# Optimization experiments

Measured on AMD Instinct MI355X. Metric: run time of the kernel, lower is better.

The kernel has to match this reference:

```python
import jax, jax.numpy as jnp
import numpy as np

N = 8192      # nodes; also input feature dim (x.shape[0] used as in_channels)
E = 524288    # edges per edge type (avg degree 64)
H = 200       # hidden dim (hard-coded in RecomNet)
MEAN_RATING = 3.5


def setup_inputs() -> dict:
    key = jax.random.key(0)
    ks = jax.random.split(key, 14)
    s_in = np.float32(1.0 / np.sqrt(N))
    s_h = np.float32(1.0 / np.sqrt(H))
    return {
        "x": jax.random.normal(ks[0], (N, N), jnp.float32),
        "edge_sim": jax.random.randint(ks[1], (2, E), 0, N),
        "edge_rat": jax.random.randint(ks[2], (2, E), 0, N),
        "mask": jax.random.randint(ks[3], (E,), 0, 2).astype(bool),
        # conv1 params (in=N, out=H)
        "w1_self": jax.random.normal(ks[4], (N, H), jnp.float32) * s_in,
        "w1_sim": jax.random.normal(ks[5], (N, H), jnp.float32) * s_in,
        "w1_rat": jax.random.normal(ks[6], (N, H), jnp.float32) * s_in,
        "b1": jnp.zeros((H,), jnp.float32),
        # conv2 params (in=H, out=H)
        "w2_self": jax.random.normal(ks[7], (H, H), jnp.float32) * s_h,
        "w2_sim": jax.random.normal(ks[8], (H, H), jnp.float32) * s_h,
        "w2_rat": jax.random.normal(ks[9], (H, H), jnp.float32) * s_h,
        "b2": jnp.zeros((H,), jnp.float32),
        # bilinear decoder
        "Q": jax.random.normal(ks[10], (H, H), jnp.float32) * s_h,
    }


def _recom_conv(edge_sim, edge_rat, x, w_self, w_sim, w_rat, b):
    # linear-then-gather-then-scatter (linear commutes with sum aggregation)
    m_sim = (x @ w_sim)[edge_sim[0]]                                   # [E, H]
    agg_sim = jax.ops.segment_sum(m_sim, edge_sim[1], num_segments=N)  # [N, H]
    m_rat = (x @ w_rat)[edge_rat[0]]
    agg_rat = jax.ops.segment_sum(m_rat, edge_rat[1], num_segments=N)
    return x @ w_self + agg_sim + agg_rat + b


def reference(x, w1_self, w1_sim, w1_rat, b1, w2_self, w2_sim, w2_rat, b2, Q,
              edge_sim, edge_rat, mask):
    h = _recom_conv(edge_sim, edge_rat, x, w1_self, w1_sim, w1_rat, b1)
    h = jax.nn.relu(h)
    h = _recom_conv(edge_sim, edge_rat, h, w2_self, w2_sim, w2_rat, b2)
    h1 = h[edge_rat[0]]                                                # [E, H]
    h2 = h[edge_rat[1]]                                                # [E, H]
    pred = jnp.einsum("eh,hk,ek->e", h1, Q, h2) + MEAN_RATING          # [E]
    # original compacts with boolean mask (dynamic shape); here we keep a
    # fixed [E] output and zero out unmasked edges
    return jnp.where(mask, pred, 0.0)
```

## Files before the change

### kernel.cpp

```cpp
#include <hip/hip_runtime.h>

#define NN 8192
#define EE 524288
#define HPAD 256
#define NP 640
#define PSS ((size_t)NN * 200)
#define PSM ((size_t)NN * 400)

using s16x8 = __attribute__((ext_vector_type(8))) short;
using u16x8 = __attribute__((ext_vector_type(8))) unsigned short;
using f32x4 = __attribute__((ext_vector_type(4))) float;

__device__ __forceinline__ unsigned short f2b(float f) {
    unsigned u = __float_as_uint(f);
    u = (u + 0x7FFFu + ((u >> 16) & 1u)) >> 16;
    return (unsigned short)u;
}
__device__ __forceinline__ float b2f(unsigned short u) {
    return __uint_as_float((unsigned)u << 16);
}
__device__ __forceinline__ unsigned pkbf16(float a, float b) {
    unsigned r;
    asm("v_cvt_pk_bf16_f32 %0, %1, %2" : "=v"(r) : "v"(a), "v"(b));
    return r;
}

__device__ __forceinline__ void async16(const unsigned short* g, unsigned short* l)
{
    __builtin_amdgcn_global_load_lds(
        (const __attribute__((address_space(1))) unsigned int*)g,
        (__attribute__((address_space(3))) unsigned int*)l, 16, 0, 0);
}

__global__ void transpose_w_kernel(
    const float* __restrict__ u0, const float* __restrict__ u1,
    const float* __restrict__ u2,
    const float* __restrict__ v0, const float* __restrict__ v1,
    const float* __restrict__ v2,
    const float* __restrict__ Q,
    unsigned short* __restrict__ o0, unsigned short* __restrict__ o1,
    unsigned short* __restrict__ o2)
{
    const int zc = blockIdx.z;
    const float *w0, *w1, *w2;
    unsigned short* out;
    int Kout, Kreal, Nreal;
    if (zc == 0)      { w0 = u0; w1 = u1; w2 = u2; out = o0; Kout = NN;   Kreal = NN;  Nreal = 600; }
    else if (zc == 1) { w0 = v0; w1 = v1; w2 = v2; out = o1; Kout = HPAD; Kreal = 200; Nreal = 600; }
    else              { w0 = Q;  w1 = Q;  w2 = Q;  out = o2; Kout = HPAD; Kreal = 200; Nreal = 200; }
    const int kb = blockIdx.x << 5;
    const int nb = blockIdx.y << 5;
    if (kb >= Kout) return;
    __shared__ float tile[32][33];
    const int tx = threadIdx.x, ty = threadIdx.y;
    const int n = nb + tx;
    const float* w = (n < 200) ? w0 : (n < 400) ? w1 : w2;
    const int c = (n < 200) ? n : (n < 400) ? n - 200 : n - 400;
#pragma unroll
    for (int i = 0; i < 4; ++i) {
        const int k = kb + ty + (i << 3);
        float v = 0.f;
        if (n < Nreal && k < Kreal) v = w[(size_t)k * 200 + c];
        tile[ty + (i << 3)][tx] = v;
    }
    __syncthreads();
#pragma unroll
    for (int i = 0; i < 4; ++i) {
        const int nn = nb + ty + (i << 3);
        out[(size_t)nn * Kout + kb + tx] = f2b(tile[tx][ty + (i << 3)]);
    }
}

template<int AF32>
__global__ __launch_bounds__(256) void gemm_mfma(
    const void* __restrict__ Araw,
    const unsigned short* __restrict__ BT,
    int lda, int KC,
    unsigned short* __restrict__ Cb, int ldc,
    float* __restrict__ ys, unsigned short* __restrict__ ysb,
    unsigned short* __restrict__ yrb,
    float* __restrict__ ysp, unsigned short* __restrict__ ymp)
{
    __shared__ unsigned short As[2][128 * 64];
    __shared__ unsigned short Bs[2][128 * 64];
    const int tid  = threadIdx.x;
    const int lane = tid & 63;
    const int w    = tid >> 6;

    const int nx   = gridDim.x;
    const int flat = blockIdx.y * nx + blockIdx.x;
    const int cpx  = (nx * gridDim.y) >> 3;
    const int orig = (flat & 7) * cpx + (flat >> 3);
    const int by   = orig / nx;
    const int bx   = orig - by * nx;

    const int row0 = by << 7;
    const int col0 = bx << 7;
    const int z    = blockIdx.z;
    const int wm = (w >> 1) << 6;
    const int wn = (w & 1) << 6;

    const int sr = lane >> 3;
    const int sc = (lane & 7) ^ sr;
    const size_t kbase = (size_t)z * KC + ((size_t)sc << 3);
    const unsigned short* bG = BT + (size_t)(col0 + w * 8 + sr) * lda + kbase;
    const int ldsOff = w * 8;

    const unsigned short* aG = nullptr;
    const float* aF = nullptr;
    int ar = 0, aq = 0;
    if constexpr (AF32) {
        ar = (w << 5) + (lane >> 2);
        aq = lane & 3;
        aF = (const float*)Araw
           + (size_t)(row0 + ar) * lda + (size_t)z * KC + aq * 16;
    } else {
        aG = (const unsigned short*)Araw
           + (size_t)(row0 + w * 8 + sr) * lda + kbase;
    }

    const f32x4 zero = {0.f, 0.f, 0.f, 0.f};
    f32x4 acc[4][4];
#pragma unroll
    for (int i = 0; i < 4; ++i)
#pragma unroll
        for (int j = 0; j < 4; ++j) acc[i][j] = zero;

    if constexpr (AF32) {
        float4 lv[8];
#pragma unroll
        for (int p_ = 0; p_ < 2; ++p_) {
            const float4* s4 = (const float4*)(aF + (size_t)(p_ * 16) * lda);
#pragma unroll
            for (int u = 0; u < 4; ++u) lv[p_ * 4 + u] = s4[u];
        }
#pragma unroll
        for (int it = 0; it < 4; ++it)
            async16(bG + (size_t)(it * 32) * lda, &Bs[0][(it * 32 + ldsOff) << 6]);
#pragma unroll
        for (int p_ = 0; p_ < 2; ++p_) {
            const int r = ar + p_ * 16;
            unsigned short* dst = &As[0][r << 6];
#pragma unroll
            for (int d = 0; d < 2; ++d) {
                const int cch = aq * 2 + d;
                const int sl  = cch ^ (r & 7);
                const float4 x0 = lv[p_ * 4 + d * 2];
                const float4 x1 = lv[p_ * 4 + d * 2 + 1];
                uint4 o;
                o.x = pkbf16(x0.x, x0.y); o.y = pkbf16(x0.z, x0.w);
                o.z = pkbf16(x1.x, x1.y); o.w = pkbf16(x1.z, x1.w);
                *(uint4*)(dst + (sl << 3)) = o;
            }
        }
    } else {
#pragma unroll
        for (int it = 0; it < 4; ++it) {
            async16(aG + (size_t)(it * 32) * lda, &As[0][(it * 32 + ldsOff) << 6]);
            async16(bG + (size_t)(it * 32) * lda, &Bs[0][(it * 32 + ldsOff) << 6]);
        }
    }
    __syncthreads();

    const int T = KC >> 6;
    for (int t = 0; t < T; ++t) {
        const int cur = t & 1;
        float4 lv[8];
        if (t + 1 < T) {
            const int ko = (t + 1) << 6;
            if constexpr (AF32) {
#pragma unroll
                for (int p_ = 0; p_ < 2; ++p_) {
                    const float4* s4 = (const float4*)(aF + (size_t)(p_ * 16) * lda + ko);
#pragma unroll
                    for (int u = 0; u < 4; ++u) lv[p_ * 4 + u] = s4[u];
                }
            } else {
#pragma unroll
                for (int it = 0; it < 4; ++it)
                    async16(aG + (size_t)(it * 32) * lda + ko,
                            &As[cur ^ 1][(it * 32 + ldsOff) << 6]);
            }
#pragma unroll
            for (int it = 0; it < 4; ++it)
                async16(bG + (size_t)(it * 32) * lda + ko,
                        &Bs[cur ^ 1][(it * 32 + ldsOff) << 6]);
        }
#pragma unroll
        for (int kk = 0; kk < 2; ++kk) {
            const int q  = (kk << 2) + (lane >> 4);
            const int sl = (q ^ (lane & 7)) << 3;
            s16x8 af[4], bfv[4];
#pragma unroll
            for (int i = 0; i < 4; ++i) {
                const int rm = wm + (i << 4) + (lane & 15);
                af[i]  = *(const s16x8*)(&As[cur][(rm << 6) + sl]);
                const int rn = wn + (i << 4) + (lane & 15);
                bfv[i] = *(const s16x8*)(&Bs[cur][(rn << 6) + sl]);
            }
#pragma unroll
            for (int i = 0; i < 4; ++i)
#pragma unroll
                for (int j = 0; j < 4; ++j)
                    acc[i][j] = __builtin_amdgcn_mfma_f32_16x16x32_bf16(
                        af[i], bfv[j], acc[i][j], 0, 0, 0);
        }
        if (t + 1 < T) {
            if constexpr (AF32) {
#pragma unroll
                for (int p_ = 0; p_ < 2; ++p_) {
                    const int r = ar + p_ * 16;
                    unsigned short* dst = &As[cur ^ 1][r << 6];
#pragma unroll
                    for (int d = 0; d < 2; ++d) {
                        const int cch = aq * 2 + d;
                        const int sl  = cch ^ (r & 7);
                        const float4 x0 = lv[p_ * 4 + d * 2];
                        const float4 x1 = lv[p_ * 4 + d * 2 + 1];
                        uint4 o;
                        o.x = pkbf16(x0.x, x0.y); o.y = pkbf16(x0.z, x0.w);
                        o.z = pkbf16(x1.x, x1.y); o.w = pkbf16(x1.z, x1.w);
                        *(uint4*)(dst + (sl << 3)) = o;
                    }
                }
            }
        }
        __syncthreads();
    }

    const int cr = (lane >> 4) << 2;
    const int cc = lane & 15;
    if (ymp) {
        float* sp = ysp + (size_t)z * PSS;
        unsigned short* mp = ymp + (size_t)z * PSM;
#pragma unroll
        for (int i = 0; i < 4; ++i)
#pragma unroll
            for (int j = 0; j < 4; ++j)
#pragma unroll
                for (int r = 0; r < 4; ++r) {
                    const int n = row0 + wm + (i << 4) + cr + r;
                    const int c = col0 + wn + (j << 4) + cc;
                    const float v = acc[i][j][r];
                    if (c < 200)      sp[(size_t)n * 200 + c] = v;
                    else if (c < 600) mp[(size_t)n * 400 + (c - 200)] = f2b(v);
                }
    } else if (ysb) {
#pragma unroll
        for (int i = 0; i < 4; ++i)
#pragma unroll
            for (int j = 0; j < 4; ++j)
#pragma unroll
                for (int r = 0; r < 4; ++r) {
                    const int n = row0 + wm + (i << 4) + cr + r;
                    const int c = col0 + wn + (j << 4) + cc;
                    const float v = acc[i][j][r];
                    if (c < 200)      ys [(size_t)n * 200 + c]        = v;
                    else if (c < 400) ysb[(size_t)n * 200 + (c - 200)] = f2b(v);
                    else if (c < 600) yrb[(size_t)n * 200 + (c - 400)] = f2b(v);
                }
    } else {
#pragma unroll
        for (int i = 0; i < 4; ++i)
#pragma unroll
            for (int j = 0; j < 4; ++j)
#pragma unroll
                for (int r = 0; r < 4; ++r)
                    Cb[(size_t)(row0 + wm + (i << 4) + cr + r) * ldc
                       + (col0 + wn + (j << 4) + cc)] = f2b(acc[i][j][r]);
    }
}

__global__ void combine_kernel(const float* __restrict__ ysp,
                               const unsigned short* __restrict__ ymp,
                               float* __restrict__ y_self,
                               unsigned short* __restrict__ y_simb,
                               unsigned short* __restrict__ y_ratb)
{
    int t = blockIdx.x * 256 + threadIdx.x;
    int n = t / 50, j4 = (t - n * 50) << 2;
    float4 s = {0.f, 0.f, 0.f, 0.f};
    float4 m = {0.f, 0.f, 0.f, 0.f};
    float4 r = {0.f, 0.f, 0.f, 0.f};
#pragma unroll
    for (int z = 0; z < 4; ++z) {
        float4 s2 = *(const float4*)(ysp + z * PSS + (size_t)n * 200 + j4);
        ushort4 m2 = *(const ushort4*)(ymp + z * PSM + (size_t)n * 400 + j4);
        ushort4 r2 = *(const ushort4*)(ymp + z * PSM + (size_t)n * 400 + 200 + j4);
        s.x += s2.x; s.y += s2.y; s.z += s2.z; s.w += s2.w;
        m.x += b2f(m2.x); m.y += b2f(m2.y); m.z += b2f(m2.z); m.w += b2f(m2.w);
        r.x += b2f(r2.x); r.y += b2f(r2.y); r.z += b2f(r2.z); r.w += b2f(r2.w);
    }
    *(float4*)(y_self + (size_t)n * 200 + j4) = s;
    ushort4 mo, ro;
    mo.x = f2b(m.x); mo.y = f2b(m.y); mo.z = f2b(m.z); mo.w = f2b(m.w);
    ro.x = f2b(r.x); ro.y = f2b(r.y); ro.z = f2b(r.z); ro.w = f2b(r.w);
    *(ushort4*)(y_simb + (size_t)n * 200 + j4) = mo;
    *(ushort4*)(y_ratb + (size_t)n * 200 + j4) = ro;
}


__global__ void hist_kernel(const int* __restrict__ e0, const int* __restrict__ e1,
                            int* __restrict__ d0, int* __restrict__ d1)
{
    const int* edges = blockIdx.y ? e1 : e0;
    int* deg = blockIdx.y ? d1 : d0;
    int e = blockIdx.x * 256 + threadIdx.x;
    if (e < EE) atomicAdd(&deg[edges[EE + e]], 1);
}

__global__ void scan_kernel(const int* __restrict__ deg0, int* __restrict__ off0,
                            int* __restrict__ pos0,
                            const int* __restrict__ deg1, int* __restrict__ off1,
                            int* __restrict__ pos1)
{
    const int* deg = blockIdx.x ? deg1 : deg0;
    int* off = blockIdx.x ? off1 : off0;
    int* pos = blockIdx.x ? pos1 : pos0;
    __shared__ int part[256];
    const int t = threadIdx.x;
    const int base = t * 32;
    int s = 0;
#pragma unroll
    for (int i = 0; i < 32; ++i) s += deg[base + i];
    part[t] = s;
    __syncthreads();
    for (int d = 1; d < 256; d <<= 1) {
        int v = (t >= d) ? part[t - d] : 0;
        __syncthreads();
        part[t] += v;
        __syncthreads();
    }
    int run = (t == 0) ? 0 : part[t - 1];
    for (int i = 0; i < 32; ++i) {
        off[base + i] = run;
        pos[base + i] = run;
        run += deg[base + i];
    }
    if (t == 255) off[NN] = run;
}

__global__ void reorder_kernel(const int* __restrict__ e0, int* __restrict__ pos0,
                               int2* __restrict__ se0,
                               const int* __restrict__ e1, int* __restrict__ pos1,
                               int2* __restrict__ se1)
{
    const int* edges = blockIdx.y ? e1 : e0;
    int* pos = blockIdx.y ? pos1 : pos0;
    int2* se = blockIdx.y ? se1 : se0;
    int e = blockIdx.x * 256 + threadIdx.x;
    if (e >= EE) return;
    int p = atomicAdd(&pos[edges[EE + e]], 1);
    se[p] = make_int2(edges[e], e);
}


__device__ __forceinline__ void edge_accum(
    const unsigned short* __restrict__ msg,
    const int* __restrict__ off, const int2* __restrict__ se,
    int n, int w, int j4, bool act, float4& acc)
{
    const int e1 = off[n + 1];
    int i = off[n] + w;
    for (; i + 12 < e1; i += 16) {
        const int s0 = se[i].x;
        const int s1 = se[i + 4].x;
        const int s2 = se[i + 8].x;
        const int s3 = se[i + 12].x;
        if (act) {
            ushort4 v0 = *(const ushort4*)(msg + (size_t)s0 * 200 + j4);
            ushort4 v1 = *(const ushort4*)(msg + (size_t)s1 * 200 + j4);
            ushort4 v2 = *(const ushort4*)(msg + (size_t)s2 * 200 + j4);
            ushort4 v3 = *(const ushort4*)(msg + (size_t)s3 * 200 + j4);
            acc.x += (b2f(v0.x) + b2f(v1.x)) + (b2f(v2.x) + b2f(v3.x));
            acc.y += (b2f(v0.y) + b2f(v1.y)) + (b2f(v2.y) + b2f(v3.y));
            acc.z += (b2f(v0.z) + b2f(v1.z)) + (b2f(v2.z) + b2f(v3.z));
            acc.w += (b2f(v0.w) + b2f(v1.w)) + (b2f(v2.w) + b2f(v3.w));
        }
    }
    for (; i < e1; i += 4) {
        const int s = se[i].x;
        if (act) {
            ushort4 v = *(const ushort4*)(msg + (size_t)s * 200 + j4);
            acc.x += b2f(v.x); acc.y += b2f(v.y);
            acc.z += b2f(v.z); acc.w += b2f(v.w);
        }
    }
}

__global__ __launch_bounds__(256) void agg_fused_kernel(
    const unsigned short* __restrict__ msg_sim,
    const unsigned short* __restrict__ msg_rat,
    const int* __restrict__ off_sim, const int2* __restrict__ se_sim,
    const int* __restrict__ off_rat, const int2* __restrict__ se_rat,
    const float* __restrict__ y_self, const float* __restrict__ bias,
    unsigned short* __restrict__ hb, int relu)
{
    __shared__ float part[4][200];
    const int n = blockIdx.x;
    const int w = threadIdx.x >> 6;
    const int lane = threadIdx.x & 63;
    const int j4 = lane << 2;
    const bool act = lane < 50;

    float4 acc = {0.f, 0.f, 0.f, 0.f};
    edge_accum(msg_sim, off_sim, se_sim, n, w, j4, act, acc);
    edge_accum(msg_rat, off_rat, se_rat, n, w, j4, act, acc);

    if (act) *(float4*)&part[w][j4] = acc;
    __syncthreads();
    const int j = threadIdx.x;
    if (j < 200) {
        float v = part[0][j] + part[1][j] + part[2][j] + part[3][j]
                + y_self[(size_t)n * 200 + j] + bias[j];
        if (relu) v = fmaxf(v, 0.f);
        hb[((size_t)n << 8) + j] = f2b(v);
    } else if (j < HPAD) {
        hb[((size_t)n << 8) + j] = 0;
    }
}

__global__ __launch_bounds__(256) void pred_kernel(
    const unsigned short* __restrict__ hQb,
    const unsigned short* __restrict__ h2b,
    const int* __restrict__ off, const int2* __restrict__ se,
    const int* __restrict__ mask, float* __restrict__ out)
{
    const int n = blockIdx.x;
    const int w = threadIdx.x >> 6;
    const int lane = threadIdx.x & 63;
    float4 b = {0.f, 0.f, 0.f, 0.f};
    if (lane < 50) {
        ushort4 v = *(const ushort4*)(h2b + ((size_t)n << 8) + (lane << 2));
        b.x = b2f(v.x); b.y = b2f(v.y); b.z = b2f(v.z); b.w = b2f(v.w);
    }
    const int e1 = off[n + 1];
    int i = off[n] + w;
    for (; i + 12 < e1; i += 16) {
        const int2 p0 = se[i];
        const int2 p1 = se[i + 4];
        const int2 p2 = se[i + 8];
        const int2 p3 = se[i + 12];
        float s0 = 0.f, s1 = 0.f, s2 = 0.f, s3 = 0.f;
        if (lane < 50) {
            ushort4 a0 = *(const ushort4*)(hQb + ((size_t)p0.x << 8) + (lane << 2));
            ushort4 a1 = *(const ushort4*)(hQb + ((size_t)p1.x << 8) + (lane << 2));
            ushort4 a2 = *(const ushort4*)(hQb + ((size_t)p2.x << 8) + (lane << 2));
            ushort4 a3 = *(const ushort4*)(hQb + ((size_t)p3.x << 8) + (lane << 2));
            s0 = fmaf(b2f(a0.x), b.x, fmaf(b2f(a0.y), b.y,
                 fmaf(b2f(a0.z), b.z, b2f(a0.w) * b.w)));
            s1 = fmaf(b2f(a1.x), b.x, fmaf(b2f(a1.y), b.y,
                 fmaf(b2f(a1.z), b.z, b2f(a1.w) * b.w)));
            s2 = fmaf(b2f(a2.x), b.x, fmaf(b2f(a2.y), b.y,
                 fmaf(b2f(a2.z), b.z, b2f(a2.w) * b.w)));
            s3 = fmaf(b2f(a3.x), b.x, fmaf(b2f(a3.y), b.y,
                 fmaf(b2f(a3.z), b.z, b2f(a3.w) * b.w)));
        }
#pragma unroll
        for (int o = 32; o > 0; o >>= 1) {
            s0 += __shfl_down(s0, o, 64);
            s1 += __shfl_down(s1, o, 64);
            s2 += __shfl_down(s2, o, 64);
            s3 += __shfl_down(s3, o, 64);
        }
        if (lane == 0) {
            out[p0.y] = mask[p0.y] ? (s0 + 3.5f) : 0.f;
            out[p1.y] = mask[p1.y] ? (s1 + 3.5f) : 0.f;
            out[p2.y] = mask[p2.y] ? (s2 + 3.5f) : 0.f;
            out[p3.y] = mask[p3.y] ? (s3 + 3.5f) : 0.f;
        }
    }
    for (; i < e1; i += 4) {
        const int2 p = se[i];
        float s = 0.f;
        if (lane < 50) {
            ushort4 a = *(const ushort4*)(hQb + ((size_t)p.x << 8) + (lane << 2));
            s = fmaf(b2f(a.x), b.x, fmaf(b2f(a.y), b.y,
                fmaf(b2f(a.z), b.z, b2f(a.w) * b.w)));
        }
#pragma unroll
        for (int o = 32; o > 0; o >>= 1) s += __shfl_down(s, o, 64);
        if (lane == 0) out[p.y] = mask[p.y] ? (s + 3.5f) : 0.f;
    }
}

extern "C" void kernel_launch(void* const* d_in, const int* in_sizes, int n_in,
                              void* d_out, int out_size, void* d_ws, size_t ws_size,
                              hipStream_t stream)
{
    const float* x       = (const float*)d_in[0];
    const int*   e_sim   = (const int*)d_in[1];
    const int*   e_rat   = (const int*)d_in[2];
    const int*   mask    = (const int*)d_in[3];
    const float* w1_self = (const float*)d_in[4];
    const float* w1_sim  = (const float*)d_in[5];
    const float* w1_rat  = (const float*)d_in[6];
    const float* b1      = (const float*)d_in[7];
    const float* w2_self = (const float*)d_in[8];
    const float* w2_sim  = (const float*)d_in[9];
    const float* w2_rat  = (const float*)d_in[10];
    const float* b2      = (const float*)d_in[11];
    const float* Q       = (const float*)d_in[12];
    float* out = (float*)d_out;

    char* p = (char*)d_ws;
    auto alloc = [&](size_t bytes) -> char* {
        char* r = p;
        p += (bytes + 255) & ~(size_t)255;
        return r;
    };
    unsigned short* wbT1  = (unsigned short*)alloc((size_t)NP * NN * 2);
    unsigned short* wbT2  = (unsigned short*)alloc((size_t)NP * HPAD * 2);
    unsigned short* QT    = (unsigned short*)alloc((size_t)HPAD * HPAD * 2);
    float* ypart_s = (float*)alloc(4 * PSS * 4);
    unsigned short* ypart_m = (unsigned short*)alloc(4 * PSM * 2);
    float* y_self = (float*)alloc((size_t)NN * 200 * 4);
    unsigned short* y_simb = (unsigned short*)alloc((size_t)NN * 200 * 2);
    unsigned short* y_ratb = (unsigned short*)alloc((size_t)NN * 200 * 2);
    unsigned short* h1b = (unsigned short*)alloc((size_t)NN * HPAD * 2);
    unsigned short* h2b = (unsigned short*)alloc((size_t)NN * HPAD * 2);
    unsigned short* hQb = (unsigned short*)alloc((size_t)NN * HPAD * 2);
    int* deg_sim = (int*)alloc(NN * 4);
    int* deg_rat = (int*)alloc(NN * 4);
    int* off_sim = (int*)alloc((NN + 1) * 4);
    int* off_rat = (int*)alloc((NN + 1) * 4);
    int* pos_sim = (int*)alloc(NN * 4);
    int* pos_rat = (int*)alloc(NN * 4);
    int2* se_sim = (int2*)alloc((size_t)EE * 8);
    int2* se_rat = (int2*)alloc((size_t)EE * 8);

    const dim3 blk(256);
    const dim3 tblk(32, 8);

    transpose_w_kernel<<<dim3(NN / 32, NP / 32, 3), tblk, 0, stream>>>(
        w1_self, w1_sim, w1_rat, w2_self, w2_sim, w2_rat, Q, wbT1, wbT2, QT);

    hipMemsetAsync(deg_sim, 0, 2 * NN * 4, stream);
    hist_kernel<<<dim3(EE / 256, 2), blk, 0, stream>>>(e_sim, e_rat, deg_sim, deg_rat);
    scan_kernel<<<2, blk, 0, stream>>>(deg_sim, off_sim, pos_sim,
                                       deg_rat, off_rat, pos_rat);
    reorder_kernel<<<dim3(EE / 256, 2), blk, 0, stream>>>(
        e_sim, pos_sim, se_sim, e_rat, pos_rat, se_rat);

    gemm_mfma<1><<<dim3(NP / 128, NN / 128, 4), blk, 0, stream>>>(
        x, wbT1, NN, NN / 4, nullptr, 0,
        nullptr, nullptr, nullptr, ypart_s, ypart_m);
    combine_kernel<<<NN * 50 / 256, blk, 0, stream>>>(
        ypart_s, ypart_m, y_self, y_simb, y_ratb);
    agg_fused_kernel<<<NN, blk, 0, stream>>>(
        y_simb, y_ratb, off_sim, se_sim, off_rat, se_rat, y_self, b1, h1b, 1);

    gemm_mfma<0><<<dim3(NP / 128, NN / 128, 1), blk, 0, stream>>>(
        h1b, wbT2, HPAD, HPAD, nullptr, 0,
        y_self, y_simb, y_ratb, nullptr, nullptr);
    agg_fused_kernel<<<NN, blk, 0, stream>>>(
        y_simb, y_ratb, off_sim, se_sim, off_rat, se_rat, y_self, b2, h2b, 0);

    gemm_mfma<0><<<dim3(HPAD / 128, NN / 128, 1), blk, 0, stream>>>(
        h2b, QT, HPAD, HPAD, hQb, HPAD,
        nullptr, nullptr, nullptr, nullptr, nullptr);
    pred_kernel<<<NN, blk, 0, stream>>>(hQb, h2b, off_rat, se_rat, mask, out);
}
```

Baseline: 803.0 us.

## Deepen fp32-A GEMM pipeline with two-stage register prefetch and manual waitcnt

For the fp32-A path of the big GEMM, loads of A are now issued two k-tiles ahead into alternating register buffers. Each tile is converted to bf16 into LDS before the MFMA phase, not after it. Explicit s_waitcnt vmcnt and raw s_barrier replace __syncthreads, so the latest A global loads can stay in flight across the barrier. The aim is to hide global load latency behind MFMA work, at the cost of more registers and fragile manual waitcnt accounting.

Result: slower. 903.2 us (+12.5%).

```diff
diff --git a/kernel.cpp b/kernel.cpp
--- a/kernel.cpp
+++ b/kernel.cpp
@@ -126,32 +126,98 @@
 #pragma unroll
         for (int j = 0; j < 4; ++j) acc[i][j] = zero;
 
+    const int T = KC >> 6;
+
     if constexpr (AF32) {
-        float4 lv[8];
-#pragma unroll
-        for (int p_ = 0; p_ < 2; ++p_) {
-            const float4* s4 = (const float4*)(aF + (size_t)(p_ * 16) * lda);
-#pragma unroll
-            for (int u = 0; u < 4; ++u) lv[p_ * 4 + u] = s4[u];
-        }
-#pragma unroll
-        for (int it = 0; it < 4; ++it)
-            async16(bG + (size_t)(it * 32) * lda, &Bs[0][(it * 32 + ldsOff) << 6]);
-#pragma unroll
-        for (int p_ = 0; p_ < 2; ++p_) {
-            const int r = ar + p_ * 16;
-            unsigned short* dst = &As[0][r << 6];
-#pragma unroll
-            for (int d = 0; d < 2; ++d) {
-                const int cch = aq * 2 + d;
-                const int sl  = cch ^ (r & 7);
-                const float4 x0 = lv[p_ * 4 + d * 2];
-                const float4 x1 = lv[p_ * 4 + d * 2 + 1];
-                uint4 o;
-                o.x = pkbf16(x0.x, x0.y); o.y = pkbf16(x0.z, x0.w);
-                o.z = pkbf16(x1.x, x1.y); o.w = pkbf16(x1.z, x1.w);
-                *(uint4*)(dst + (sl << 3)) = o;
-            }
+        auto loadA = [&](float4 (&dst)[8], int ko) __attribute__((always_inline)) {
+#pragma unroll
+            for (int p_ = 0; p_ < 2; ++p_) {
+                const float4* s4 = (const float4*)(aF + (size_t)(p_ * 16) * lda + ko);
+#pragma unroll
+                for (int u = 0; u < 4; ++u) dst[p_ * 4 + u] = s4[u];
+            }
+        };
+        auto convA = [&](float4 (&src)[8], int buf) __attribute__((always_inline)) {
+#pragma unroll
+            for (int p_ = 0; p_ < 2; ++p_) {
+                const int r = ar + p_ * 16;
+                unsigned short* dst = &As[buf][r << 6];
+#pragma unroll
+                for (int d = 0; d < 2; ++d) {
+                    const int cch = aq * 2 + d;
+                    const int sl  = cch ^ (r & 7);
+                    const float4 x0 = src[p_ * 4 + d * 2];
+                    const float4 x1 = src[p_ * 4 + d * 2 + 1];
+                    uint4 o;
+                    o.x = pkbf16(x0.x, x0.y); o.y = pkbf16(x0.z, x0.w);
+                    o.z = pkbf16(x1.x, x1.y); o.w = pkbf16(x1.z, x1.w);
+                    *(uint4*)(dst + (sl << 3)) = o;
+                }
+            }
+        };
+        auto dmaB = [&](int ko, int buf) __attribute__((always_inline)) {
+#pragma unroll
+            for (int it = 0; it < 4; ++it)
+                async16(bG + (size_t)(it * 32) * lda + ko,
+                        &Bs[buf][(it * 32 + ldsOff) << 6]);
+        };
+        auto mfmaPhase = [&](int buf) __attribute__((always_inline)) {
+#pragma unroll
+            for (int kk = 0; kk < 2; ++kk) {
+                const int q  = (kk << 2) + (lane >> 4);
+                const int sl = (q ^ (lane & 7)) << 3;
+                s16x8 af[4], bfv[4];
+#pragma unroll
+                for (int i = 0; i < 4; ++i) {
+                    const int rm = wm + (i << 4) + (lane & 15);
+                    af[i]  = *(const s16x8*)(&As[buf][(rm << 6) + sl]);
+                    const int rn = wn + (i << 4) + (lane & 15);
+                    bfv[i] = *(const s16x8*)(&Bs[buf][(rn << 6) + sl]);
+                }
+#pragma unroll
+                for (int i = 0; i < 4; ++i)
+#pragma unroll
+                    for (int j = 0; j < 4; ++j)
+                        acc[i][j] = __builtin_amdgcn_mfma_f32_16x16x32_bf16(
+                            af[i], bfv[j], acc[i][j], 0, 0, 0);
+            }
+        };
+
+        float4 lvA[8], lvB[8];
+        loadA(lvA, 0);
+        dmaB(0, 0);
+        convA(lvA, 0);
+        __builtin_amdgcn_sched_barrier(0);
+        if (T > 1) {
+            loadA(lvB, 64);
+            asm volatile("s_waitcnt vmcnt(8) lgkmcnt(0)" ::: "memory");
+        } else {
+            asm volatile("s_waitcnt vmcnt(0) lgkmcnt(0)" ::: "memory");
+        }
+        __builtin_amdgcn_s_barrier();
+
+        auto step = [&](int t, float4 (&use)[8], float4 (&fill)[8])
+            __attribute__((always_inline)) {
+            const int cur = t & 1;
+            if (t + 1 < T) {
+                dmaB((t + 1) << 6, cur ^ 1);
+                convA(use, cur ^ 1);
+            }
+            __builtin_amdgcn_sched_barrier(0);
+            if (t + 2 < T)
+                loadA(fill, (t + 2) << 6);
+            mfmaPhase(cur);
+            if (t + 1 < T) {
+                if (t + 2 < T)
+                    asm volatile("s_waitcnt vmcnt(8) lgkmcnt(0)" ::: "memory");
+                else
+                    asm volatile("s_waitcnt vmcnt(0) lgkmcnt(0)" ::: "memory");
+                __builtin_amdgcn_s_barrier();
+            }
+        };
+        for (int t = 0; t < T; t += 2) {
+            step(t,     lvB, lvA);
+            step(t + 1, lvA, lvB);
         }
     } else {
 #pragma unroll
@@ -159,73 +225,40 @@
             async16(aG + (size_t)(it * 32) * lda, &As[0][(it * 32 + ldsOff) << 6]);
             async16(bG + (size_t)(it * 32) * lda, &Bs[0][(it * 32 + ldsOff) << 6]);
         }
-    }
-    __syncthreads();
-
-    const int T = KC >> 6;
-    for (int t = 0; t < T; ++t) {
-        const int cur = t & 1;
-        float4 lv[8];
-        if (t + 1 < T) {
-            const int ko = (t + 1) << 6;
-            if constexpr (AF32) {
-#pragma unroll
-                for (int p_ = 0; p_ < 2; ++p_) {
-                    const float4* s4 = (const float4*)(aF + (size_t)(p_ * 16) * lda + ko);
-#pragma unroll
-                    for (int u = 0; u < 4; ++u) lv[p_ * 4 + u] = s4[u];
-                }
-            } else {
-#pragma unroll
-                for (int it = 0; it < 4; ++it)
+        __syncthreads();
+        for (int t = 0; t < T; ++t) {
+            const int cur = t & 1;
+            if (t + 1 < T) {
+                const int ko = (t + 1) << 6;
+#pragma unroll
+                for (int it = 0; it < 4; ++it) {
                     async16(aG + (size_t)(it * 32) * lda + ko,
                             &As[cur ^ 1][(it * 32 + ldsOff) << 6]);
-            }
-#pragma unroll
-            for (int it = 0; it < 4; ++it)
-                async16(bG + (size_t)(it * 32) * lda + ko,
-                        &Bs[cur ^ 1][(it * 32 + ldsOff) << 6]);
-        }
-#pragma unroll
-        for (int kk = 0; kk < 2; ++kk) {
-            const int q  = (kk << 2) + (lane >> 4);
-            const int sl = (q ^ (lane & 7)) << 3;
-            s16x8 af[4], bfv[4];
-#pragma unroll
-            for (int i = 0; i < 4; ++i) {
-                const int rm = wm + (i << 4) + (lane & 15);
-                af[i]  = *(const s16x8*)(&As[cur][(rm << 6) + sl]);
-                const int rn = wn + (i << 4) + (lane & 15);
-                bfv[i] = *(const s16x8*)(&Bs[cur][(rn << 6) + sl]);
-            }
-#pragma unroll
-            for (int i = 0; i < 4; ++i)
-#pragma unroll
-                for (int j = 0; j < 4; ++j)
-                    acc[i][j] = __builtin_amdgcn_mfma_f32_16x16x32_bf16(
-                        af[i], bfv[j], acc[i][j], 0, 0, 0);
-        }
-        if (t + 1 < T) {
-            if constexpr (AF32) {
-#pragma unroll
-                for (int p_ = 0; p_ < 2; ++p_) {
-                    const int r = ar + p_ * 16;
-                    unsigned short* dst = &As[cur ^ 1][r << 6];
-#pragma unroll
-                    for (int d = 0; d < 2; ++d) {
-                        const int cch = aq * 2 + d;
-                        const int sl  = cch ^ (r & 7);
-                        const float4 x0 = lv[p_ * 4 + d * 2];
-                        const float4 x1 = lv[p_ * 4 + d * 2 + 1];
-                        uint4 o;
-                        o.x = pkbf16(x0.x, x0.y); o.y = pkbf16(x0.z, x0.w);
-                        o.z = pkbf16(x1.x, x1.y); o.w = pkbf16(x1.z, x1.w);
-                        *(uint4*)(dst + (sl << 3)) = o;
-                    }
+                    async16(bG + (size_t)(it * 32) * lda + ko,
+                            &Bs[cur ^ 1][(it * 32 + ldsOff) << 6]);
                 }
             }
-        }
-        __syncthreads();
+#pragma unroll
+            for (int kk = 0; kk < 2; ++kk) {
+                const int q  = (kk << 2) + (lane >> 4);
+                const int sl = (q ^ (lane & 7)) << 3;
+                s16x8 af[4], bfv[4];
+#pragma unroll
+                for (int i = 0; i < 4; ++i) {
+                    const int rm = wm + (i << 4) + (lane & 15);
+                    af[i]  = *(const s16x8*)(&As[cur][(rm << 6) + sl]);
+                    const int rn = wn + (i << 4) + (lane & 15);
+                    bfv[i] = *(const s16x8*)(&Bs[cur][(rn << 6) + sl]);
+                }
+#pragma unroll
+                for (int i = 0; i < 4; ++i)
+#pragma unroll
+                    for (int j = 0; j < 4; ++j)
+                        acc[i][j] = __builtin_amdgcn_mfma_f32_16x16x32_bf16(
+                            af[i], bfv[j], acc[i][j], 0, 0, 0);
+            }
+            __syncthreads();
+        }
     }
 
     const int cr = (lane >> 4) << 2;
```

## Use 512-thread blocks in MFMA GEMM with 8 waves per 128x128 tile

Applied to the files above, without the earlier changes.

Doubles the GEMM block size from 4 to 8 wavefronts. Each wave now computes a 32x64 sub-tile (2x4 MFMA fragments) instead of 64x64, which halves per-thread accumulators and the fp32 A-staging registers. Global-to-LDS loads are redistributed so each thread handles half as many rows. The aim is more resident waves to hide memory latency in the large x@W GEMM, at the cost of more LDS fragment reads per MFMA and more synchronisation overhead per block.

After: 811.8 us. No clear change (+1.1%).

```diff
diff --git a/kernel.cpp b/kernel.cpp
--- a/kernel.cpp
+++ b/kernel.cpp
@@ -72,7 +72,7 @@
 }
 
 template<int AF32>
-__global__ __launch_bounds__(256) void gemm_mfma(
+__global__ __launch_bounds__(512) void gemm_mfma(
     const void* __restrict__ Araw,
     const unsigned short* __restrict__ BT,
     int lda, int KC,
@@ -97,8 +97,8 @@
     const int row0 = by << 7;
     const int col0 = bx << 7;
     const int z    = blockIdx.z;
-    const int wm = (w >> 1) << 6;
-    const int wn = (w & 1) << 6;
+    const int wm = (w & 3) << 5;
+    const int wn = (w >> 2) << 6;
 
     const int sr = lane >> 3;
     const int sc = (lane & 7) ^ sr;
@@ -110,8 +110,8 @@
     const float* aF = nullptr;
     int ar = 0, aq = 0;
     if constexpr (AF32) {
-        ar = (w << 5) + (lane >> 2);
-        aq = lane & 3;
+        ar = tid >> 2;
+        aq = tid & 3;
         aF = (const float*)Araw
            + (size_t)(row0 + ar) * lda + (size_t)z * KC + aq * 16;
     } else {
@@ -120,112 +120,121 @@
     }
 
     const f32x4 zero = {0.f, 0.f, 0.f, 0.f};
-    f32x4 acc[4][4];
-#pragma unroll
-    for (int i = 0; i < 4; ++i)
+    f32x4 acc[2][4];
+#pragma unroll
+    for (int i = 0; i < 2; ++i)
 #pragma unroll
         for (int j = 0; j < 4; ++j) acc[i][j] = zero;
 
+    const int T = KC >> 6;
+
     if constexpr (AF32) {
-        float4 lv[8];
-#pragma unroll
-        for (int p_ = 0; p_ < 2; ++p_) {
-            const float4* s4 = (const float4*)(aF + (size_t)(p_ * 16) * lda);
-#pragma unroll
-            for (int u = 0; u < 4; ++u) lv[p_ * 4 + u] = s4[u];
-        }
-#pragma unroll
-        for (int it = 0; it < 4; ++it)
-            async16(bG + (size_t)(it * 32) * lda, &Bs[0][(it * 32 + ldsOff) << 6]);
-#pragma unroll
-        for (int p_ = 0; p_ < 2; ++p_) {
-            const int r = ar + p_ * 16;
-            unsigned short* dst = &As[0][r << 6];
+        float4 lv[4];
+        auto loadA = [&](int ko) __attribute__((always_inline)) {
+            const float4* s4 = (const float4*)(aF + ko);
+#pragma unroll
+            for (int u = 0; u < 4; ++u) lv[u] = s4[u];
+        };
+        auto convA = [&](int buf) __attribute__((always_inline)) {
+            unsigned short* dst = &As[buf][ar << 6];
 #pragma unroll
             for (int d = 0; d < 2; ++d) {
                 const int cch = aq * 2 + d;
-                const int sl  = cch ^ (r & 7);
-                const float4 x0 = lv[p_ * 4 + d * 2];
-                const float4 x1 = lv[p_ * 4 + d * 2 + 1];
+                const int sl  = cch ^ (ar & 7);
+                const float4 x0 = lv[d * 2];
+                const float4 x1 = lv[d * 2 + 1];
                 uint4 o;
                 o.x = pkbf16(x0.x, x0.y); o.y = pkbf16(x0.z, x0.w);
                 o.z = pkbf16(x1.x, x1.y); o.w = pkbf16(x1.z, x1.w);
                 *(uint4*)(dst + (sl << 3)) = o;
             }
+        };
+        loadA(0);
+#pragma unroll
+        for (int it = 0; it < 2; ++it)
+            async16(bG + (size_t)(it * 64) * lda, &Bs[0][(it * 64 + ldsOff) << 6]);
+        convA(0);
+        __syncthreads();
+
+        for (int t = 0; t < T; ++t) {
+            const int cur = t & 1;
+            if (t + 1 < T) {
+                const int ko = (t + 1) << 6;
+                loadA(ko);
+#pragma unroll
+                for (int it = 0; it < 2; ++it)
+                    async16(bG + (size_t)(it * 64) * lda + ko,
+                            &Bs[cur ^ 1][(it * 64 + ldsOff) << 6]);
+            }
+#pragma unroll
+            for (int kk = 0; kk < 2; ++kk) {
+                const int q  = (kk << 2) + (lane >> 4);
+                const int sl = (q ^ (lane & 7)) << 3;
+                s16x8 af[2], bfv[4];
+#pragma unroll
+                for (int i = 0; i < 2; ++i) {
+                    const int rm = wm + (i << 4) + (lane & 15);
+                    af[i] = *(const s16x8*)(&As[cur][(rm << 6) + sl]);
+                }
+#pragma unroll
+                for (int j = 0; j < 4; ++j) {
+                    const int rn = wn + (j << 4) + (lane & 15);
+                    bfv[j] = *(const s16x8*)(&Bs[cur][(rn << 6) + sl]);
+                }
+#pragma unroll
+                for (int i = 0; i < 2; ++i)
+#pragma unroll
+                    for (int j = 0; j < 4; ++j)
+                        acc[i][j] = __builtin_amdgcn_mfma_f32_16x16x32_bf16(
+                            af[i], bfv[j], acc[i][j], 0, 0, 0);
+            }
+            if (t + 1 < T)
+                convA(cur ^ 1);
+            __syncthreads();
         }
     } else {
 #pragma unroll
-        for (int it = 0; it < 4; ++it) {
-            async16(aG + (size_t)(it * 32) * lda, &As[0][(it * 32 + ldsOff) << 6]);
-            async16(bG + (size_t)(it * 32) * lda, &Bs[0][(it * 32 + ldsOff) << 6]);
-        }
-    }
-    __syncthreads();
-
-    const int T = KC >> 6;
-    for (int t = 0; t < T; ++t) {
-        const int cur = t & 1;
-        float4 lv[8];
-        if (t + 1 < T) {
-            const int ko = (t + 1) << 6;
-            if constexpr (AF32) {
-#pragma unroll
-                for (int p_ = 0; p_ < 2; ++p_) {
-                    const float4* s4 = (const float4*)(aF + (size_t)(p_ * 16) * lda + ko);
-#pragma unroll
-                    for (int u = 0; u < 4; ++u) lv[p_ * 4 + u] = s4[u];
-                }
-            } else {
-#pragma unroll
-                for (int it = 0; it < 4; ++it)
-                    async16(aG + (size_t)(it * 32) * lda + ko,
-                            &As[cur ^ 1][(it * 32 + ldsOff) << 6]);
+        for (int it = 0; it < 2; ++it) {
+            async16(aG + (size_t)(it * 64) * lda, &As[0][(it * 64 + ldsOff) << 6]);
+            async16(bG + (size_t)(it * 64) * lda, &Bs[0][(it * 64 + ldsOff) << 6]);
+        }
+        __syncthreads();
+        for (int t = 0; t < T; ++t) {
+            const int cur = t & 1;
+            if (t + 1 < T) {
+                const int ko = (t + 1) << 6;
+#pragma unroll
+                for (int it = 0; it < 2; ++it) {
+                    async16(aG + (size_t)(it * 64) * lda + ko,
+                            &As[cur ^ 1][(it * 64 + ldsOff) << 6]);
+                    async16(bG + (size_t)(it * 64) * lda + ko,
+                            &Bs[cur ^ 1][(it * 64 + ldsOff) << 6]);
+                }
             }
 #pragma unroll
-            for (int it = 0; it < 4; ++it)
-                async16(bG + (size_t)(it * 32) * lda + ko,
-                        &Bs[cur ^ 1][(it * 32 + ldsOff) << 6]);
-        }
-#pragma unroll
-        for (int kk = 0; kk < 2; ++kk) {
-            const int q  = (kk << 2) + (lane >> 4);
-            const int sl = (q ^ (lane & 7)) << 3;
-            s16x8 af[4], bfv[4];
-#pragma unroll
-            for (int i = 0; i < 4; ++i) {
-                const int rm = wm + (i << 4) + (lane & 15);
-                af[i]  = *(const s16x8*)(&As[cur][(rm << 6) + sl]);
-                const int rn = wn + (i << 4) + (lane & 15);
-                bfv[i] = *(const s16x8*)(&Bs[cur][(rn << 6) + sl]);
+            for (int kk = 0; kk < 2; ++kk) {
+                const int q  = (kk << 2) + (lane >> 4);
+                const int sl = (q ^ (lane & 7)) << 3;
+                s16x8 af[2], bfv[4];
+#pragma unroll
+                for (int i = 0; i < 2; ++i) {
+                    const int rm = wm + (i << 4) + (lane & 15);
+                    af[i] = *(const s16x8*)(&As[cur][(rm << 6) + sl]);
+                }
+#pragma unroll
+                for (int j = 0; j < 4; ++j) {
+                    const int rn = wn + (j << 4) + (lane & 15);
+                    bfv[j] = *(const s16x8*)(&Bs[cur][(rn << 6) + sl]);
+                }
+#pragma unroll
+                for (int i = 0; i < 2; ++i)
+#pragma unroll
+                    for (int j = 0; j < 4; ++j)
+                        acc[i][j] = __builtin_amdgcn_mfma_f32_16x16x32_bf16(
+                            af[i], bfv[j], acc[i][j], 0, 0, 0);
             }
-#pragma unroll
-            for (int i = 0; i < 4; ++i)
-#pragma unroll
-                for (int j = 0; j < 4; ++j)
-                    acc[i][j] = __builtin_amdgcn_mfma_f32_16x16x32_bf16(
-                        af[i], bfv[j], acc[i][j], 0, 0, 0);
-        }
-        if (t + 1 < T) {
-            if constexpr (AF32) {
-#pragma unroll
-                for (int p_ = 0; p_ < 2; ++p_) {
-                    const int r = ar + p_ * 16;
-                    unsigned short* dst = &As[cur ^ 1][r << 6];
-#pragma unroll
-                    for (int d = 0; d < 2; ++d) {
-                        const int cch = aq * 2 + d;
-                        const int sl  = cch ^ (r & 7);
-                        const float4 x0 = lv[p_ * 4 + d * 2];
-                        const float4 x1 = lv[p_ * 4 + d * 2 + 1];
-                        uint4 o;
-                        o.x = pkbf16(x0.x, x0.y); o.y = pkbf16(x0.z, x0.w);
-                        o.z = pkbf16(x1.x, x1.y); o.w = pkbf16(x1.z, x1.w);
-                        *(uint4*)(dst + (sl << 3)) = o;
-                    }
-                }
-            }
-        }
-        __syncthreads();
+            __syncthreads();
+        }
     }
 
     const int cr = (lane >> 4) << 2;
@@ -234,7 +243,7 @@
         float* sp = ysp + (size_t)z * PSS;
         unsigned short* mp = ymp + (size_t)z * PSM;
 #pragma unroll
-        for (int i = 0; i < 4; ++i)
+        for (int i = 0; i < 2; ++i)
 #pragma unroll
             for (int j = 0; j < 4; ++j)
 #pragma unroll
@@ -247,7 +256,7 @@
                 }
     } else if (ysb) {
 #pragma unroll
-        for (int i = 0; i < 4; ++i)
+        for (int i = 0; i < 2; ++i)
 #pragma unroll
             for (int j = 0; j < 4; ++j)
 #pragma unroll
@@ -261,7 +270,7 @@
                 }
     } else {
 #pragma unroll
-        for (int i = 0; i < 4; ++i)
+        for (int i = 0; i < 2; ++i)
 #pragma unroll
             for (int j = 0; j < 4; ++j)
 #pragma unroll
@@ -530,6 +539,7 @@
     int2* se_rat = (int2*)alloc((size_t)EE * 8);
 
     const dim3 blk(256);
+    const dim3 gblk(512);
     const dim3 tblk(32, 8);
 
     transpose_w_kernel<<<dim3(NN / 32, NP / 32, 3), tblk, 0, stream>>>(
@@ -542,7 +552,7 @@
     reorder_kernel<<<dim3(EE / 256, 2), blk, 0, stream>>>(
         e_sim, pos_sim, se_sim, e_rat, pos_rat, se_rat);
 
-    gemm_mfma<1><<<dim3(NP / 128, NN / 128, 4), blk, 0, stream>>>(
+    gemm_mfma<1><<<dim3(NP / 128, NN / 128, 4), gblk, 0, stream>>>(
         x, wbT1, NN, NN / 4, nullptr, 0,
         nullptr, nullptr, nullptr, ypart_s, ypart_m);
     combine_kernel<<<NN * 50 / 256, blk, 0, stream>>>(
@@ -550,13 +560,13 @@
     agg_fused_kernel<<<NN, blk, 0, stream>>>(
         y_simb, y_ratb, off_sim, se_sim, off_rat, se_rat, y_self, b1, h1b, 1);
 
-    gemm_mfma<0><<<dim3(NP / 128, NN / 128, 1), blk, 0, stream>>>(
+    gemm_mfma<0><<<dim3(NP / 128, NN / 128, 1), gblk, 0, stream>>>(
         h1b, wbT2, HPAD, HPAD, nullptr, 0,
         y_self, y_simb, y_ratb, nullptr, nullptr);
     agg_fused_kernel<<<NN, blk, 0, stream>>>(
         y_simb, y_ratb, off_sim, se_sim, off_rat, se_rat, y_self, b2, h2b, 0);
 
-    gemm_mfma<0><<<dim3(HPAD / 128, NN / 128, 1), blk, 0, stream>>>(
+    gemm_mfma<0><<<dim3(HPAD / 128, NN / 128, 1), gblk, 0, stream>>>(
         h2b, QT, HPAD, HPAD, hQb, HPAD,
         nullptr, nullptr, nullptr, nullptr, nullptr);
     pred_kernel<<<NN, blk, 0, stream>>>(hQb, h2b, off_rat, se_rat, mask, out);
```
